# Performance work log

Measured on AMD Instinct MI355X. Metric: run time of the kernel, lower is better.

Reference implementation:

```python
import jax, jax.numpy as jnp
import numpy as np

EPS = 1e-5

def _fftfreq(n, d):
    k = jnp.concatenate([jnp.arange(0, (n + 1) // 2), jnp.arange(-(n // 2), 0)]).astype(jnp.float32)
    return k / (n * d)

def _inorm(x):
    # InstanceNorm2d, no affine, biased variance, eps=1e-5; x: (B,C,H,W)
    m = jnp.mean(x, axis=(-2, -1), keepdims=True)
    v = jnp.var(x, axis=(-2, -1), keepdims=True)
    return (x - m) / jnp.sqrt(v + EPS)

def _spectral_conv(x, t_grid, x_grid, p1, p2, res):
    # x: (B, C, Sx, Sy) real; p1:(in,out,m1) p2:(in,out,m2) res:(in,out,m1,m2) complex64
    B, C, Sx, Sy = x.shape
    dty = x_grid[0, 1] - x_grid[0, 0]
    dtx = t_grid[0, 1] - t_grid[0, 0]
    alpha = jnp.fft.fft2(x, axes=(-2, -1))  # (B,in,Sx,Sy) complex
    om1 = (_fftfreq(Sx, dty) * (2 * jnp.pi) * 1j).astype(jnp.complex64)  # (Sx,)
    om2 = (_fftfreq(Sy, dtx) * (2 * jnp.pi) * 1j).astype(jnp.complex64)  # (Sy,)
    d1 = om1[:, None, None, None] - p1  # (Sx,in,out,m1)
    d2 = om2[:, None, None, None] - p2  # (Sy,in,out,m2)
    denom = jnp.einsum('pbix,qbik->pqbixk', d1, d2)  # (Sx,Sy,in,out,m1,m2)
    Hw = res[None, None] / denom  # pole-residue rational kernel
    r1 = jnp.einsum('biox,oxikpq->bkox', alpha, Hw)  # (B,out,Sx,Sy)
    r2 = jnp.einsum('biox,oxikpq->bkpq', alpha, Hw)  # (B,out,m1,m2)
    x1 = jnp.real(jnp.fft.ifft2(r1, s=(Sx, Sy), axes=(-2, -1)))
    ty_c = x_grid.reshape(1, -1).astype(jnp.complex64)  # (1,Sx)
    tx_c = t_grid.reshape(1, -1).astype(jnp.complex64)  # (1,Sy)
    e1 = jnp.exp(jnp.einsum('bip,kz->bipz', p1, ty_c))  # (in,out,m1,Sx)
    e2 = jnp.exp(jnp.einsum('biq,kx->biqx', p2, tx_c))  # (in,out,m2,Sy)
    term3 = jnp.einsum('bipz,biqx->bipqzx', e1, e2)     # (in,out,m1,m2,Sx,Sy)
    x2 = jnp.real(jnp.einsum('kbpq,bipqzx->kizx', r2, term3)) / (Sx * Sy)
    return x1 + x2

def reference(x, fc0_w, fc0_b, p1r, p1i, p2r, p2i, resr, resi,
              w0_w, w0_b, fc1_w, fc1_b, fc2_w, fc2_b, t_grid, x_grid):
    B, Sx, Sy, _ = x.shape
    gx = jnp.broadcast_to(jnp.linspace(0.0, 1.0, Sx, dtype=jnp.float32)[None, :, None, None], (B, Sx, Sy, 1))
    gy = jnp.broadcast_to(jnp.linspace(0.0, 1.0, Sy, dtype=jnp.float32)[None, None, :, None], (B, Sx, Sy, 1))
    h = jnp.concatenate([x, gx, gy], axis=-1)           # (B,Sx,Sy,3)
    h = h @ fc0_w.T + fc0_b                              # (B,Sx,Sy,16)
    h = h.transpose(0, 3, 1, 2)                          # (B,16,Sx,Sy)
    p1 = (p1r + 1j * p1i).astype(jnp.complex64)
    p2 = (p2r + 1j * p2i).astype(jnp.complex64)
    res = (resr + 1j * resi).astype(jnp.complex64)
    x1 = _inorm(_spectral_conv(_inorm(h), t_grid, x_grid, p1, p2, res))
    x2 = jnp.einsum('bihw,oi->bohw', h, w0_w) + w0_b[None, :, None, None]  # 1x1 conv
    h = x1 + x2
    h = h.transpose(0, 2, 3, 1)                          # (B,Sx,Sy,16)
    h = jnp.sin(h @ fc1_w.T + fc1_b)                     # (B,Sx,Sy,128)
    h = h @ fc2_w.T + fc2_b                              # (B,Sx,Sy,1)
    return h

def setup_inputs() -> dict:
    key = jax.random.key(0)
    ks = jax.random.split(key, 16)
    W, M1, M2, B, S = 16, 4, 5, 4, 64
    scale = 1.0 / (W * W)
    inp = {
        'x': jax.random.normal(ks[0], (B, S, S, 1), jnp.float32),
        'fc0_w': jax.random.normal(ks[1], (W, 3), jnp.float32) * 0.3,
        'fc0_b': jax.random.normal(ks[2], (W,), jnp.float32) * 0.1,
        'p1r': jax.random.uniform(ks[3], (W, W, M1), jnp.float32) * scale,
        'p1i': jax.random.uniform(ks[4], (W, W, M1), jnp.float32) * scale,
        'p2r': jax.random.uniform(ks[5], (W, W, M2), jnp.float32) * scale,
        'p2i': jax.random.uniform(ks[6], (W, W, M2), jnp.float32) * scale,
        'resr': jax.random.uniform(ks[7], (W, W, M1, M2), jnp.float32) * scale,
        'resi': jax.random.uniform(ks[8], (W, W, M1, M2), jnp.float32) * scale,
        'w0_w': jax.random.normal(ks[9], (W, W), jnp.float32) * 0.25,
        'w0_b': jax.random.normal(ks[10], (W,), jnp.float32) * 0.1,
        'fc1_w': jax.random.normal(ks[11], (128, W), jnp.float32) * 0.25,
        'fc1_b': jax.random.normal(ks[12], (128,), jnp.float32) * 0.1,
        'fc2_w': jax.random.normal(ks[13], (1, 128), jnp.float32) * 0.1,
        'fc2_b': jax.random.normal(ks[14], (1,), jnp.float32) * 0.1,
        't_grid': jnp.linspace(0.0, 1.0, S, dtype=jnp.float32).reshape(1, S),
        'x_grid': jnp.linspace(0.0, 1.0, S, dtype=jnp.float32).reshape(1, S),
    }
    return inp
```

## Files before the change

### kernel.cpp

```cpp
#include <hip/hip_runtime.h>

typedef float2 cplx;

constexpr float TWO_PI = 6.28318530717958647692f;

__device__ inline void cmac(float& ax, float& ay, cplx a, cplx b) {
    ax += a.x * b.x - a.y * b.y;
    ay += a.x * b.y + a.y * b.x;
}

__global__ __launch_bounds__(256) void k_pre(
    const float* __restrict__ x, const float* __restrict__ fc0_w,
    const float* __restrict__ fc0_b,
    const float* __restrict__ p1r, const float* __restrict__ p1i,
    const float* __restrict__ p2r, const float* __restrict__ p2i,
    const float* __restrict__ resr, const float* __restrict__ resi,
    const float* __restrict__ t_grid, const float* __restrict__ x_grid,
    cplx* __restrict__ A, cplx* __restrict__ Bq, cplx* __restrict__ Cq,
    cplx* __restrict__ e1, cplx* __restrict__ e2,
    float* __restrict__ h, float* __restrict__ accH2)
{
    int idx = blockIdx.x * 256 + threadIdx.x;
    float dty = x_grid[1] - x_grid[0];
    float dtx = t_grid[1] - t_grid[0];
    const int NA = 65536, NBQ = 81920, NCQ = 81920, NE1 = 65536, NE2 = 81920;
    if (idx < NA) {
        int p = idx & 3, k = (idx >> 2) & 15, i = (idx >> 6) & 15, o = idx >> 10;
        int kf = (o < 32) ? o : o - 64;
        float om = TWO_PI * (float)kf / (64.f * dty);
        float dr = -p1r[(i * 16 + k) * 4 + p], di = om - p1i[(i * 16 + k) * 4 + p];
        float inv = 1.f / (dr * dr + di * di);
        A[idx] = make_float2(dr * inv, -di * inv);
        return;
    }
    idx -= NA;
    if (idx < NBQ) {
        int q = idx % 5, k = (idx / 5) & 15, i = (idx / 80) & 15, xx = idx / 1280;
        int kf = (xx < 32) ? xx : xx - 64;
        float om = TWO_PI * (float)kf / (64.f * dtx);
        float dr = -p2r[(i * 16 + k) * 5 + q], di = om - p2i[(i * 16 + k) * 5 + q];
        float inv = 1.f / (dr * dr + di * di);
        Bq[idx] = make_float2(dr * inv, -di * inv);
        return;
    }
    idx -= NBQ;
    if (idx < NCQ) {
        int q = idx % 5, k = (idx / 5) & 15, i = (idx / 80) & 15, o = idx / 1280;
        int kf = (o < 32) ? o : o - 64;
        float om = TWO_PI * (float)kf / (64.f * dty);
        float cx = 0.f, cy = 0.f;
        for (int p = 0; p < 4; ++p) {
            float dr = -p1r[(i * 16 + k) * 4 + p], di = om - p1i[(i * 16 + k) * 4 + p];
            float inv = 1.f / (dr * dr + di * di);
            float axr = dr * inv, axi = -di * inv;
            float rr = resr[((i * 16 + k) * 4 + p) * 5 + q];
            float ri = resi[((i * 16 + k) * 4 + p) * 5 + q];
            cx += rr * axr - ri * axi;
            cy += rr * axi + ri * axr;
        }
        Cq[idx] = make_float2(cx, cy);
        return;
    }
    idx -= NCQ;
    if (idx < NE1) {
        int z = idx & 63, w = idx >> 6;
        float t = x_grid[z];
        float m = expf(p1r[w] * t);
        float sn, cs; sincosf(p1i[w] * t, &sn, &cs);
        e1[idx] = make_float2(m * cs, m * sn);
        return;
    }
    idx -= NE1;
    if (idx < NE2) {
        int xx = idx & 63, w = idx >> 6;
        float t = t_grid[xx];
        float m = expf(p2r[w] * t);
        float sn, cs; sincosf(p2i[w] * t, &sn, &cs);
        e2[idx] = make_float2(m * cs, m * sn);
        return;
    }
    idx -= NE2;
    {
        int bc = idx >> 12, pix = idx & 4095;
        int b = bc >> 4, c = bc & 15;
        int z = pix >> 6, xx = pix & 63;
        const float inv63 = 1.f / 63.f;
        float v = fc0_w[c * 3] * x[b * 4096 + pix]
                + fc0_w[c * 3 + 1] * (z * inv63)
                + fc0_w[c * 3 + 2] * (xx * inv63) + fc0_b[c];
        h[idx] = v;
        float s = v, s2 = v * v;
        for (int m = 32; m; m >>= 1) {
            s  += __shfl_xor(s,  m, 64);
            s2 += __shfl_xor(s2, m, 64);
        }
        if ((threadIdx.x & 63) == 0) {
            int widx = pix >> 6;
            accH2[bc * 128 + widx * 2]     = s;
            accH2[bc * 128 + widx * 2 + 1] = s2;
        }
    }
}

__global__ __launch_bounds__(256) void kFFT(
    const float* __restrict__ h, const float* __restrict__ accH2,
    cplx* __restrict__ alpha, cplx* __restrict__ alphaT)
{
    __shared__ float hs[4096];
    __shared__ cplx  T1s[512];
    __shared__ cplx  Ws[64];
    __shared__ float mv[2];
    int bc = blockIdx.x >> 3, pg = blockIdx.x & 7;
    int tid = threadIdx.x;
    if (tid < 64) { float sn, cs; sincosf(-TWO_PI * tid / 64.f, &sn, &cs); Ws[tid] = make_float2(cs, sn); }
    else if (tid < 128) {
        int l = tid - 64;
        float s  = accH2[bc * 128 + l * 2];
        float s2 = accH2[bc * 128 + l * 2 + 1];
        for (int m = 32; m; m >>= 1) { s += __shfl_xor(s, m, 64); s2 += __shfl_xor(s2, m, 64); }
        if (l == 0) {
            float mean = s * (1.f / 4096.f);
            float var  = s2 * (1.f / 4096.f) - mean * mean;
            mv[0] = mean; mv[1] = rsqrtf(var + 1e-5f);
        }
    }
    for (int t = 0; t < 16; ++t) hs[t * 256 + tid] = h[bc * 4096 + t * 256 + tid];
    __syncthreads();
    float mean = mv[0], rstd = mv[1];
    for (int t = 0; t < 2; ++t) {
        int idx = t * 256 + tid;
        int pl = idx >> 6, j = idx & 63;
        int p = pg * 8 + pl;
        float ax0 = 0.f, ay0 = 0.f, ax1 = 0.f, ay1 = 0.f;
        #pragma unroll
        for (int i = 0; i < 64; i += 2) {
            float v0 = hs[i * 64 + j];       cplx w0 = Ws[(p * i) & 63];
            ax0 += v0 * w0.x; ay0 += v0 * w0.y;
            float v1 = hs[(i + 1) * 64 + j]; cplx w1 = Ws[(p * (i + 1)) & 63];
            ax1 += v1 * w1.x; ay1 += v1 * w1.y;
        }
        float ax = ax0 + ax1, ay = ay0 + ay1;
        if (p == 0) ax -= 64.f * mean;
        T1s[pl * 64 + j] = make_float2(ax * rstd, ay * rstd);
    }
    __syncthreads();
    for (int t = 0; t < 2; ++t) {
        int idx = t * 256 + tid;
        int pl = idx >> 6, q = idx & 63;
        int p = pg * 8 + pl;
        float ax0 = 0.f, ay0 = 0.f, ax1 = 0.f, ay1 = 0.f;
        const cplx* trow = &T1s[pl * 64];
        #pragma unroll
        for (int j = 0; j < 64; j += 2) {
            cmac(ax0, ay0, trow[j],     Ws[(q * j) & 63]);
            cmac(ax1, ay1, trow[j + 1], Ws[(q * (j + 1)) & 63]);
        }
        cplx v = make_float2(ax0 + ax1, ay0 + ay1);
        alpha [bc * 4096 + p * 64 + q] = v;
        alphaT[(p * 64 + q) * 64 + bc] = v;
    }
}

__global__ __launch_bounds__(64) void k3_r1(
    const cplx* __restrict__ alphaT, const cplx* __restrict__ Cq,
    const cplx* __restrict__ Bq, cplx* __restrict__ r1)
{
    __shared__ cplx Cqs[1280], Bqs[1280], Gs[256], as[64];
    int ox = blockIdx.x; int o = ox >> 6, xx = ox & 63;
    int t = threadIdx.x;
    for (int m = 0; m < 20; ++m) {
        Cqs[m * 64 + t] = Cq[o * 1280 + m * 64 + t];
        Bqs[m * 64 + t] = Bq[xx * 1280 + m * 64 + t];
    }
    as[t] = alphaT[ox * 64 + t];
    __syncthreads();
    for (int m = 0; m < 4; ++m) {
        int e = m * 64 + t; int i = e >> 4, k = e & 15;
        float gx = 0.f, gy = 0.f;
        for (int q = 0; q < 5; ++q) cmac(gx, gy, Cqs[i * 80 + k * 5 + q], Bqs[i * 80 + k * 5 + q]);
        Gs[e] = make_float2(gx, gy);
    }
    __syncthreads();
    int b = t >> 4, k = t & 15;
    float ax0 = 0.f, ay0 = 0.f, ax1 = 0.f, ay1 = 0.f;
    #pragma unroll
    for (int i = 0; i < 16; i += 2) {
        cmac(ax0, ay0, as[b * 16 + i],     Gs[i * 16 + k]);
        cmac(ax1, ay1, as[b * 16 + i + 1], Gs[(i + 1) * 16 + k]);
    }
    r1[t * 4096 + ox] = make_float2(ax0 + ax1, ay0 + ay1);
}

__global__ __launch_bounds__(1024) void k45_r2(
    const cplx* __restrict__ alpha, const cplx* __restrict__ Bq,
    const cplx* __restrict__ A,
    const float* __restrict__ resr, const float* __restrict__ resi,
    cplx* __restrict__ r2)
{
    __shared__ cplx red[16][20];
    int bk = blockIdx.x; int b = bk >> 4, k = bk & 15;
    int o = threadIdx.x & 63, i = threadIdx.x >> 6;
    float inx[5] = {}, iny[5] = {};
    const cplx* arow = alpha + (b * 16 + i) * 4096 + o * 64;
    const cplx* bq   = Bq + i * 80 + k * 5;
    #pragma unroll 4
    for (int xx = 0; xx < 64; ++xx) {
        cplx av = arow[xx];
        const cplx* bv = bq + xx * 1280;
        for (int q = 0; q < 5; ++q) {
            inx[q] += av.x * bv[q].x - av.y * bv[q].y;
            iny[q] += av.x * bv[q].y + av.y * bv[q].x;
        }
    }
    float accx[4][5], accy[4][5];
    int rb = (i * 16 + k) * 20;
    for (int p = 0; p < 4; ++p) {
        cplx a = A[((o * 16 + i) * 16 + k) * 4 + p];
        for (int q = 0; q < 5; ++q) {
            float tx = a.x * inx[q] - a.y * iny[q];
            float ty = a.x * iny[q] + a.y * inx[q];
            float rr = resr[rb + p * 5 + q], ri = resi[rb + p * 5 + q];
            accx[p][q] = rr * tx - ri * ty;
            accy[p][q] = rr * ty + ri * tx;
        }
    }
    for (int m = 32; m; m >>= 1)
        for (int p = 0; p < 4; ++p)
            for (int q = 0; q < 5; ++q) {
                accx[p][q] += __shfl_xor(accx[p][q], m, 64);
                accy[p][q] += __shfl_xor(accy[p][q], m, 64);
            }
    if (o == 0)
        for (int p = 0; p < 4; ++p)
            for (int q = 0; q < 5; ++q)
                red[i][p * 5 + q] = make_float2(accx[p][q], accy[p][q]);
    __syncthreads();
    if (threadIdx.x < 20) {
        float sx = 0.f, sy = 0.f;
        for (int g = 0; g < 16; ++g) { sx += red[g][threadIdx.x].x; sy += red[g][threadIdx.x].y; }
        r2[bk * 20 + threadIdx.x] = make_float2(sx, sy);
    }
}

__global__ __launch_bounds__(256) void k78_sp(
    const cplx* __restrict__ r1, const cplx* __restrict__ r2,
    const cplx* __restrict__ e1, const cplx* __restrict__ e2,
    float* __restrict__ sp, float* __restrict__ accS2)
{
    __shared__ cplx rs[4096];
    __shared__ cplx T2s[512];
    __shared__ cplx Vs[640];
    __shared__ cplx Ws[64];
    int bc = blockIdx.x >> 3, zg = blockIdx.x & 7;
    int b = bc >> 4, ch = bc & 15;
    int tid = threadIdx.x;
    if (tid < 64) { float sn, cs; sincosf(TWO_PI * tid / 64.f, &sn, &cs); Ws[tid] = make_float2(cs, sn); }
    for (int t = 0; t < 16; ++t) rs[t * 256 + tid] = r1[bc * 4096 + t * 256 + tid];
    for (int e = tid; e < 640; e += 256) {
        int zl = e & 7, bq = e >> 3;
        int bb = bq / 5, q = bq - bb * 5;
        int z = zg * 8 + zl;
        float vx = 0.f, vy = 0.f;
        for (int p = 0; p < 4; ++p)
            cmac(vx, vy, r2[(b * 16 + bb) * 20 + p * 5 + q],
                         e1[((bb * 16 + ch) * 4 + p) * 64 + z]);
        Vs[bq * 8 + zl] = make_float2(vx, vy);
    }
    __syncthreads();
    for (int t = 0; t < 2; ++t) {
        int idx = t * 256 + tid;
        int zl = idx >> 6, j = idx & 63;
        int z = zg * 8 + zl;
        float ax0 = 0.f, ay0 = 0.f, ax1 = 0.f, ay1 = 0.f;
        #pragma unroll
        for (int o = 0; o < 64; o += 2) {
            cmac(ax0, ay0, rs[o * 64 + j],       Ws[(z * o) & 63]);
            cmac(ax1, ay1, rs[(o + 1) * 64 + j], Ws[(z * (o + 1)) & 63]);
        }
        T2s[zl * 64 + j] = make_float2(ax0 + ax1, ay0 + ay1);
    }
    __syncthreads();
    float s = 0.f, s2 = 0.f;
    for (int t = 0; t < 2; ++t) {
        int lp = t * 256 + tid;
        int zl = lp >> 6, xx = lp & 63;
        float ax0 = 0.f, ax1 = 0.f;
        const cplx* trow = &T2s[zl * 64];
        #pragma unroll
        for (int j = 0; j < 64; j += 2) {
            cplx v0 = trow[j];     cplx w0 = Ws[(xx * j) & 63];
            ax0 += v0.x * w0.x - v0.y * w0.y;
            cplx v1 = trow[j + 1]; cplx w1 = Ws[(xx * (j + 1)) & 63];
            ax1 += v1.x * w1.x - v1.y * w1.y;
        }
        float acc = ax0 + ax1;
        const cplx* eb = e2 + ch * 320 + xx;
        #pragma unroll 4
        for (int bb = 0; bb < 16; ++bb)
            for (int q = 0; q < 5; ++q) {
                cplx vv = Vs[(bb * 5 + q) * 8 + zl];
                cplx ee = eb[bb * 5120 + q * 64];
                acc += vv.x * ee.x - vv.y * ee.y;
            }
        float val = acc * (1.f / 4096.f);
        sp[bc * 4096 + zg * 512 + lp] = val;
        s += val; s2 += val * val;
    }
    for (int m = 32; m; m >>= 1) {
        s  += __shfl_xor(s,  m, 64);
        s2 += __shfl_xor(s2, m, 64);
    }
    if ((tid & 63) == 0) {
        int widx = zg * 4 + (tid >> 6);
        accS2[bc * 64 + widx * 2]     = s;
        accS2[bc * 64 + widx * 2 + 1] = s2;
    }
}

__global__ __launch_bounds__(256) void k9_final(
    const float* __restrict__ sp, const float* __restrict__ accS2,
    const float* __restrict__ h,
    const float* __restrict__ w0_w, const float* __restrict__ w0_b,
    const float* __restrict__ fc1_w, const float* __restrict__ fc1_b,
    const float* __restrict__ fc2_w, const float* __restrict__ fc2_b,
    float* __restrict__ out)
{
    __shared__ float w1s[128 * 16], b1s[128], w2s[128], w0s[256], w0bs[16];
    __shared__ float mvm[16], mvr[16];
    int tid = threadIdx.x;
    int b = blockIdx.x >> 4;
    for (int t = 0; t < 8; ++t) w1s[t * 256 + tid] = fc1_w[t * 256 + tid];
    if (tid < 128) { b1s[tid] = fc1_b[tid]; w2s[tid] = fc2_w[tid]; }
    w0s[tid] = w0_w[tid & 255];
    if (tid < 16) w0bs[tid] = w0_b[tid];
    {
        int wv = tid >> 6, ln = tid & 63;
        for (int cc = 0; cc < 4; ++cc) {
            int c = wv * 4 + cc;
            float s = 0.f, s2 = 0.f;
            if (ln < 32) {
                s  = accS2[(b * 16 + c) * 64 + ln * 2];
                s2 = accS2[(b * 16 + c) * 64 + ln * 2 + 1];
            }
            for (int m = 16; m; m >>= 1) { s += __shfl_xor(s, m, 64); s2 += __shfl_xor(s2, m, 64); }
            if (ln == 0) {
                float mean = s * (1.f / 4096.f);
                float var  = s2 * (1.f / 4096.f) - mean * mean;
                mvm[c] = mean; mvr[c] = rsqrtf(var + 1e-5f);
            }
        }
    }
    float b2 = fc2_b[0];
    __syncthreads();
    int pix = blockIdx.x * 256 + tid;
    int rem = pix & 4095;
    float hv[16], tv[16];
    for (int c = 0; c < 16; ++c) {
        hv[c] = h[(b * 16 + c) * 4096 + rem];
        tv[c] = (sp[(b * 16 + c) * 4096 + rem] - mvm[c]) * mvr[c];
    }
    for (int k = 0; k < 16; ++k) {
        float a = w0bs[k];
        for (int c = 0; c < 16; ++c) a += w0s[k * 16 + c] * hv[c];
        tv[k] += a;
    }
    float acc = b2;
    for (int n = 0; n < 128; ++n) {
        float s1 = b1s[n];
        for (int k2 = 0; k2 < 16; ++k2) s1 += w1s[n * 16 + k2] * tv[k2];
        acc += w2s[n] * sinf(s1);
    }
    out[pix] = acc;
}

extern "C" void kernel_launch(void* const* d_in, const int* in_sizes, int n_in,
                              void* d_out, int out_size, void* d_ws, size_t ws_size,
                              hipStream_t stream)
{
    const float* x     = (const float*)d_in[0];
    const float* fc0_w = (const float*)d_in[1];
    const float* fc0_b = (const float*)d_in[2];
    const float* p1r   = (const float*)d_in[3];
    const float* p1i   = (const float*)d_in[4];
    const float* p2r   = (const float*)d_in[5];
    const float* p2i   = (const float*)d_in[6];
    const float* resr  = (const float*)d_in[7];
    const float* resi  = (const float*)d_in[8];
    const float* w0_w  = (const float*)d_in[9];
    const float* w0_b  = (const float*)d_in[10];
    const float* fc1_w = (const float*)d_in[11];
    const float* fc1_b = (const float*)d_in[12];
    const float* fc2_w = (const float*)d_in[13];
    const float* fc2_b = (const float*)d_in[14];
    const float* t_grid= (const float*)d_in[15];
    const float* x_grid= (const float*)d_in[16];
    float* out = (float*)d_out;

    float* ws = (float*)d_ws;
    size_t off = 0;
    float* h      = ws + off; off += 262144;
    cplx*  alpha  = (cplx*)(ws + off); off += 524288;
    cplx*  alphaT = (cplx*)(ws + off); off += 524288;
    cplx*  A      = (cplx*)(ws + off); off += 131072;
    cplx*  Bq     = (cplx*)(ws + off); off += 163840;
    cplx*  Cq     = (cplx*)(ws + off); off += 163840;
    cplx*  e1     = (cplx*)(ws + off); off += 131072;
    cplx*  e2     = (cplx*)(ws + off); off += 163840;
    cplx*  r1     = (cplx*)(ws + off); off += 524288;
    cplx*  r2     = (cplx*)(ws + off); off += 2560;
    float* sp     = ws + off; off += 262144;
    float* accH2  = ws + off; off += 8192;
    float* accS2  = ws + off; off += 4096;
    (void)ws_size; (void)n_in; (void)in_sizes; (void)out_size;

    k_pre<<<2496, 256, 0, stream>>>(x, fc0_w, fc0_b, p1r, p1i, p2r, p2i, resr, resi,
                                    t_grid, x_grid, A, Bq, Cq, e1, e2, h, accH2);
    kFFT<<<512, 256, 0, stream>>>(h, accH2, alpha, alphaT);
    k3_r1<<<4096, 64, 0, stream>>>(alphaT, Cq, Bq, r1);
    k45_r2<<<64, 1024, 0, stream>>>(alpha, Bq, A, resr, resi, r2);
    k78_sp<<<512, 256, 0, stream>>>(r1, r2, e1, e2, sp, accS2);
    k9_final<<<64, 256, 0, stream>>>(sp, accS2, h, w0_w, w0_b, fc1_w, fc1_b, fc2_w, fc2_b, out);
}
```

Measured before the change: 208.9 us.

## Reorder r2 contraction loops and add transposed Bq for coalesced loads

The r2 kernel now makes each lane own one column index and loops over the row index. It accumulates alpha times the A factor per pole p first, then applies Bq per lane from a new transposed BqT buffer. Before, each lane walked a contiguous row of alpha with a large stride into Bq. The new order gives coalesced alpha loads and lane-contiguous BqT reads. It costs an extra transposed copy of Bq written in the precompute kernel and more workspace.

```diff
diff --git a/kernel.cpp b/kernel.cpp
--- a/kernel.cpp
+++ b/kernel.cpp
@@ -16,7 +16,8 @@
     const float* __restrict__ p2r, const float* __restrict__ p2i,
     const float* __restrict__ resr, const float* __restrict__ resi,
     const float* __restrict__ t_grid, const float* __restrict__ x_grid,
-    cplx* __restrict__ A, cplx* __restrict__ Bq, cplx* __restrict__ Cq,
+    cplx* __restrict__ A, cplx* __restrict__ Bq, cplx* __restrict__ BqT,
+    cplx* __restrict__ Cq,
     cplx* __restrict__ e1, cplx* __restrict__ e2,
     float* __restrict__ h, float* __restrict__ accH2)
 {
@@ -40,7 +41,9 @@
         float om = TWO_PI * (float)kf / (64.f * dtx);
         float dr = -p2r[(i * 16 + k) * 5 + q], di = om - p2i[(i * 16 + k) * 5 + q];
         float inv = 1.f / (dr * dr + di * di);
-        Bq[idx] = make_float2(dr * inv, -di * inv);
+        cplx v = make_float2(dr * inv, -di * inv);
+        Bq[idx] = v;
+        BqT[((i * 16 + k) * 5 + q) * 64 + xx] = v;
         return;
     }
     idx -= NBQ;
@@ -191,49 +194,50 @@
     r1[t * 4096 + ox] = make_float2(ax0 + ax1, ay0 + ay1);
 }
 
-__global__ __launch_bounds__(1024) void k45_r2(
-    const cplx* __restrict__ alpha, const cplx* __restrict__ Bq,
-    const cplx* __restrict__ A,
+__global__ __launch_bounds__(1024) void k5c_r2(
+    const cplx* __restrict__ alpha, const cplx* __restrict__ A,
+    const cplx* __restrict__ BqT,
     const float* __restrict__ resr, const float* __restrict__ resi,
     cplx* __restrict__ r2)
 {
     __shared__ cplx red[16][20];
     int bk = blockIdx.x; int b = bk >> 4, k = bk & 15;
-    int o = threadIdx.x & 63, i = threadIdx.x >> 6;
-    float inx[5] = {}, iny[5] = {};
-    const cplx* arow = alpha + (b * 16 + i) * 4096 + o * 64;
-    const cplx* bq   = Bq + i * 80 + k * 5;
-    #pragma unroll 4
-    for (int xx = 0; xx < 64; ++xx) {
-        cplx av = arow[xx];
-        const cplx* bv = bq + xx * 1280;
-        for (int q = 0; q < 5; ++q) {
-            inx[q] += av.x * bv[q].x - av.y * bv[q].y;
-            iny[q] += av.x * bv[q].y + av.y * bv[q].x;
-        }
-    }
-    float accx[4][5], accy[4][5];
+    int lane = threadIdx.x & 63, i = threadIdx.x >> 6;
+    float w1x[4] = {}, w1y[4] = {};
+    const cplx* arow  = alpha + (b * 16 + i) * 4096 + lane;
+    const cplx* Abase = A + (i * 16 + k) * 4;
+    #pragma unroll 8
+    for (int o = 0; o < 64; ++o) {
+        cplx av = arow[o * 64];
+        const cplx* ao = Abase + o * 1024;
+        for (int p = 0; p < 4; ++p) {
+            w1x[p] += ao[p].x * av.x - ao[p].y * av.y;
+            w1y[p] += ao[p].x * av.y + ao[p].y * av.x;
+        }
+    }
+    float ox[4][5], oy[4][5];
+    const cplx* bqt = BqT + (i * 16 + k) * 320 + lane;
     int rb = (i * 16 + k) * 20;
-    for (int p = 0; p < 4; ++p) {
-        cplx a = A[((o * 16 + i) * 16 + k) * 4 + p];
-        for (int q = 0; q < 5; ++q) {
-            float tx = a.x * inx[q] - a.y * iny[q];
-            float ty = a.x * iny[q] + a.y * inx[q];
+    for (int q = 0; q < 5; ++q) {
+        cplx bv = bqt[q * 64];
+        for (int p = 0; p < 4; ++p) {
+            float tx = w1x[p] * bv.x - w1y[p] * bv.y;
+            float ty = w1x[p] * bv.y + w1y[p] * bv.x;
             float rr = resr[rb + p * 5 + q], ri = resi[rb + p * 5 + q];
-            accx[p][q] = rr * tx - ri * ty;
-            accy[p][q] = rr * ty + ri * tx;
+            ox[p][q] = rr * tx - ri * ty;
+            oy[p][q] = rr * ty + ri * tx;
         }
     }
     for (int m = 32; m; m >>= 1)
         for (int p = 0; p < 4; ++p)
             for (int q = 0; q < 5; ++q) {
-                accx[p][q] += __shfl_xor(accx[p][q], m, 64);
-                accy[p][q] += __shfl_xor(accy[p][q], m, 64);
+                ox[p][q] += __shfl_xor(ox[p][q], m, 64);
+                oy[p][q] += __shfl_xor(oy[p][q], m, 64);
             }
-    if (o == 0)
+    if (lane == 0)
         for (int p = 0; p < 4; ++p)
             for (int q = 0; q < 5; ++q)
-                red[i][p * 5 + q] = make_float2(accx[p][q], accy[p][q]);
+                red[i][p * 5 + q] = make_float2(ox[p][q], oy[p][q]);
     __syncthreads();
     if (threadIdx.x < 20) {
         float sx = 0.f, sy = 0.f;
@@ -403,6 +407,7 @@
     cplx*  alphaT = (cplx*)(ws + off); off += 524288;
     cplx*  A      = (cplx*)(ws + off); off += 131072;
     cplx*  Bq     = (cplx*)(ws + off); off += 163840;
+    cplx*  BqT    = (cplx*)(ws + off); off += 163840;
     cplx*  Cq     = (cplx*)(ws + off); off += 163840;
     cplx*  e1     = (cplx*)(ws + off); off += 131072;
     cplx*  e2     = (cplx*)(ws + off); off += 163840;
@@ -414,10 +419,10 @@
     (void)ws_size; (void)n_in; (void)in_sizes; (void)out_size;
 
     k_pre<<<2496, 256, 0, stream>>>(x, fc0_w, fc0_b, p1r, p1i, p2r, p2i, resr, resi,
-                                    t_grid, x_grid, A, Bq, Cq, e1, e2, h, accH2);
+                                    t_grid, x_grid, A, Bq, BqT, Cq, e1, e2, h, accH2);
     kFFT<<<512, 256, 0, stream>>>(h, accH2, alpha, alphaT);
     k3_r1<<<4096, 64, 0, stream>>>(alphaT, Cq, Bq, r1);
-    k45_r2<<<64, 1024, 0, stream>>>(alpha, Bq, A, resr, resi, r2);
+    k5c_r2<<<64, 1024, 0, stream>>>(alpha, A, BqT, resr, resi, r2);
     k78_sp<<<512, 256, 0, stream>>>(r1, r2, e1, e2, sp, accS2);
     k9_final<<<64, 256, 0, stream>>>(sp, accS2, h, w0_w, w0_b, fc1_w, fc1_b, fc2_w, fc2_b, out);
 }
```

After: 223.8 us. +7.1%, slower.

## Split r2 computation into inner-product and reduction kernels, pack k3_r1 blocks

Applied to the files above, without the earlier changes.

The r2 path used 64 blocks of 1024 threads, each doing a 64-step inner product plus a shuffle reduction. It is now split into a highly parallel k4_inner1 kernel that writes an intermediate buffer and a k5d_r2 kernel that reduces per (b,i,k) and accumulates into r2 with atomics, after a memset. k3_r1 now packs four 64-thread work items per 256-thread block and reads Cq/Bq directly from global memory instead of staging them in shared memory. This aims to fix the low occupancy of the old r2 kernel, at the cost of an extra launch, an intermediate global buffer, and atomics whose float summation order is nondeterministic.

```diff
diff --git a/kernel.cpp b/kernel.cpp
--- a/kernel.cpp
+++ b/kernel.cpp
@@ -161,84 +161,87 @@
     }
 }
 
-__global__ __launch_bounds__(64) void k3_r1(
+__global__ __launch_bounds__(256) void k3_r1(
     const cplx* __restrict__ alphaT, const cplx* __restrict__ Cq,
     const cplx* __restrict__ Bq, cplx* __restrict__ r1)
 {
-    __shared__ cplx Cqs[1280], Bqs[1280], Gs[256], as[64];
-    int ox = blockIdx.x; int o = ox >> 6, xx = ox & 63;
-    int t = threadIdx.x;
-    for (int m = 0; m < 20; ++m) {
-        Cqs[m * 64 + t] = Cq[o * 1280 + m * 64 + t];
-        Bqs[m * 64 + t] = Bq[xx * 1280 + m * 64 + t];
-    }
-    as[t] = alphaT[ox * 64 + t];
-    __syncthreads();
+    __shared__ cplx Gs[4][256];
+    __shared__ cplx as[4][64];
+    int w = threadIdx.x >> 6, t = threadIdx.x & 63;
+    int ox = blockIdx.x * 4 + w;
+    int o = ox >> 6, xx = ox & 63;
+    as[w][t] = alphaT[ox * 64 + t];
+    const cplx* cq = Cq + o * 1280;
+    const cplx* bq = Bq + xx * 1280;
     for (int m = 0; m < 4; ++m) {
-        int e = m * 64 + t; int i = e >> 4, k = e & 15;
+        int e = m * 64 + t;
         float gx = 0.f, gy = 0.f;
-        for (int q = 0; q < 5; ++q) cmac(gx, gy, Cqs[i * 80 + k * 5 + q], Bqs[i * 80 + k * 5 + q]);
-        Gs[e] = make_float2(gx, gy);
+        #pragma unroll
+        for (int q = 0; q < 5; ++q) cmac(gx, gy, cq[e * 5 + q], bq[e * 5 + q]);
+        Gs[w][e] = make_float2(gx, gy);
     }
     __syncthreads();
     int b = t >> 4, k = t & 15;
     float ax0 = 0.f, ay0 = 0.f, ax1 = 0.f, ay1 = 0.f;
     #pragma unroll
     for (int i = 0; i < 16; i += 2) {
-        cmac(ax0, ay0, as[b * 16 + i],     Gs[i * 16 + k]);
-        cmac(ax1, ay1, as[b * 16 + i + 1], Gs[(i + 1) * 16 + k]);
+        cmac(ax0, ay0, as[w][b * 16 + i],     Gs[w][i * 16 + k]);
+        cmac(ax1, ay1, as[w][b * 16 + i + 1], Gs[w][(i + 1) * 16 + k]);
     }
     r1[t * 4096 + ox] = make_float2(ax0 + ax1, ay0 + ay1);
 }
 
-__global__ __launch_bounds__(1024) void k45_r2(
+__global__ __launch_bounds__(256) void k4_inner1(
     const cplx* __restrict__ alpha, const cplx* __restrict__ Bq,
-    const cplx* __restrict__ A,
+    cplx* __restrict__ inner1)
+{
+    int idx = blockIdx.x * 256 + threadIdx.x;
+    int kq = idx % 80; int r = idx / 80; int o = r & 63; int bi = r >> 6; int i = bi & 15;
+    const cplx* arow = alpha + bi * 4096 + o * 64;
+    const cplx* bcol = Bq + i * 80 + kq;
+    float ax = 0.f, ay = 0.f;
+    #pragma unroll 4
+    for (int x = 0; x < 64; ++x) cmac(ax, ay, arow[x], bcol[x * 1280]);
+    inner1[idx] = make_float2(ax, ay);
+}
+
+__global__ __launch_bounds__(64) void k5d_r2(
+    const cplx* __restrict__ inner1, const cplx* __restrict__ A,
     const float* __restrict__ resr, const float* __restrict__ resi,
     cplx* __restrict__ r2)
 {
-    __shared__ cplx red[16][20];
-    int bk = blockIdx.x; int b = bk >> 4, k = bk & 15;
-    int o = threadIdx.x & 63, i = threadIdx.x >> 6;
-    float inx[5] = {}, iny[5] = {};
-    const cplx* arow = alpha + (b * 16 + i) * 4096 + o * 64;
-    const cplx* bq   = Bq + i * 80 + k * 5;
-    #pragma unroll 4
-    for (int xx = 0; xx < 64; ++xx) {
-        cplx av = arow[xx];
-        const cplx* bv = bq + xx * 1280;
+    int blk = blockIdx.x;
+    int k = blk & 15, i = (blk >> 4) & 15, b = blk >> 8;
+    int o = threadIdx.x;
+    cplx in[5];
+    const cplx* ip = inner1 + (b * 16 + i) * 5120 + o * 80 + k * 5;
+    #pragma unroll
+    for (int q = 0; q < 5; ++q) in[q] = ip[q];
+    float ox[4][5], oy[4][5];
+    int rb = (i * 16 + k) * 20;
+    const cplx* ap = A + ((o * 16 + i) * 16 + k) * 4;
+    #pragma unroll
+    for (int p = 0; p < 4; ++p) {
+        cplx a = ap[p];
+        #pragma unroll
         for (int q = 0; q < 5; ++q) {
-            inx[q] += av.x * bv[q].x - av.y * bv[q].y;
-            iny[q] += av.x * bv[q].y + av.y * bv[q].x;
-        }
-    }
-    float accx[4][5], accy[4][5];
-    int rb = (i * 16 + k) * 20;
-    for (int p = 0; p < 4; ++p) {
-        cplx a = A[((o * 16 + i) * 16 + k) * 4 + p];
-        for (int q = 0; q < 5; ++q) {
-            float tx = a.x * inx[q] - a.y * iny[q];
-            float ty = a.x * iny[q] + a.y * inx[q];
+            float tx = a.x * in[q].x - a.y * in[q].y;
+            float ty = a.x * in[q].y + a.y * in[q].x;
             float rr = resr[rb + p * 5 + q], ri = resi[rb + p * 5 + q];
-            accx[p][q] = rr * tx - ri * ty;
-            accy[p][q] = rr * ty + ri * tx;
+            ox[p][q] = rr * tx - ri * ty;
+            oy[p][q] = rr * ty + ri * tx;
         }
     }
     for (int m = 32; m; m >>= 1)
         for (int p = 0; p < 4; ++p)
             for (int q = 0; q < 5; ++q) {
-                accx[p][q] += __shfl_xor(accx[p][q], m, 64);
-                accy[p][q] += __shfl_xor(accy[p][q], m, 64);
+                ox[p][q] += __shfl_xor(ox[p][q], m, 64);
+                oy[p][q] += __shfl_xor(oy[p][q], m, 64);
             }
-    if (o == 0)
-        for (int p = 0; p < 4; ++p)
-            for (int q = 0; q < 5; ++q)
-                red[i][p * 5 + q] = make_float2(accx[p][q], accy[p][q]);
-    __syncthreads();
-    if (threadIdx.x < 20) {
-        float sx = 0.f, sy = 0.f;
-        for (int g = 0; g < 16; ++g) { sx += red[g][threadIdx.x].x; sy += red[g][threadIdx.x].y; }
-        r2[bk * 20 + threadIdx.x] = make_float2(sx, sy);
+    if (o < 20) {
+        int p = o / 5, q = o % 5;
+        atomicAdd(&r2[(b * 16 + k) * 20 + o].x, ox[p][q]);
+        atomicAdd(&r2[(b * 16 + k) * 20 + o].y, oy[p][q]);
     }
 }
 
@@ -407,17 +410,21 @@
     cplx*  e1     = (cplx*)(ws + off); off += 131072;
     cplx*  e2     = (cplx*)(ws + off); off += 163840;
     cplx*  r1     = (cplx*)(ws + off); off += 524288;
+    cplx*  inner1 = (cplx*)(ws + off); off += 655360;
     cplx*  r2     = (cplx*)(ws + off); off += 2560;
     float* sp     = ws + off; off += 262144;
     float* accH2  = ws + off; off += 8192;
     float* accS2  = ws + off; off += 4096;
     (void)ws_size; (void)n_in; (void)in_sizes; (void)out_size;
 
+    hipMemsetAsync(r2, 0, 1280 * sizeof(cplx), stream);
+
     k_pre<<<2496, 256, 0, stream>>>(x, fc0_w, fc0_b, p1r, p1i, p2r, p2i, resr, resi,
                                     t_grid, x_grid, A, Bq, Cq, e1, e2, h, accH2);
     kFFT<<<512, 256, 0, stream>>>(h, accH2, alpha, alphaT);
-    k3_r1<<<4096, 64, 0, stream>>>(alphaT, Cq, Bq, r1);
-    k45_r2<<<64, 1024, 0, stream>>>(alpha, Bq, A, resr, resi, r2);
+    k3_r1<<<1024, 256, 0, stream>>>(alphaT, Cq, Bq, r1);
+    k4_inner1<<<1280, 256, 0, stream>>>(alpha, Bq, inner1);
+    k5d_r2<<<1024, 64, 0, stream>>>(inner1, A, resr, resi, r2);
     k78_sp<<<512, 256, 0, stream>>>(r1, r2, e1, e2, sp, accS2);
     k9_final<<<64, 256, 0, stream>>>(sp, accS2, h, w0_w, w0_b, fc1_w, fc1_b, fc2_w, fc2_b, out);
 }
```

Measured after the change: 211.4 us. Within noise of the previous version (+1.2%).
